# Performance work log

Measured on AMD Instinct MI355X. Metric: run time of the kernel, lower is better.

The kernel has to match this reference:

```python
import jax, jax.numpy as jnp
import numpy as np

LEAKY_SLOPE = 0.01  # torch nn.LeakyReLU default

def leaky_relu(x):
    return jnp.where(x >= 0, x, LEAKY_SLOPE * x)

def setup_inputs() -> dict:
    key = jax.random.key(0)
    ks = jax.random.split(key, 11)
    B, F, C_IN, H, K, D = 2048, 512, 3, 64, 8, 128  # batch, features, expand, layer_conf[0], bucket_num, bucket_dim
    ASR, MM, OUT = 128, 768, 256
    proj_in = ASR + MM + F * D
    inp = {
        "stat_features": jax.random.uniform(ks[0], (B, F), dtype=jnp.float32),
        "asr_embeddings": jax.random.normal(ks[1], (B, ASR), dtype=jnp.float32),
        "mm_embeddings": jax.random.normal(ks[2], (B, MM), dtype=jnp.float32),
        "linear1_w": jax.random.normal(ks[3], (F, C_IN, H), dtype=jnp.float32) * (1.0 / np.sqrt(C_IN)),
        "linear1_b": jax.random.normal(ks[4], (F, 1, H), dtype=jnp.float32),
        "linear2_w": jax.random.normal(ks[5], (F, H, K), dtype=jnp.float32) * (1.0 / np.sqrt(H)),
        "linear2_b": jax.random.normal(ks[6], (F, 1, K), dtype=jnp.float32),
        "tau": jnp.ones((F, 1, K), dtype=jnp.float32),
        "emb": jax.random.normal(ks[7], (F, K, D), dtype=jnp.float32),
        "proj_w": jax.random.normal(ks[8], (OUT, proj_in), dtype=jnp.float32) * (1.0 / np.sqrt(proj_in)),
        "proj_b": jax.random.normal(ks[9], (OUT,), dtype=jnp.float32) * 0.01,
    }
    return inp

def reference(stat_features, asr_embeddings, mm_embeddings,
              linear1_w, linear1_b, linear2_w, linear2_b, tau, emb,
              proj_w, proj_b):
    # sanitize: NaN -> 0, negatives -> 0
    x = stat_features
    x = jnp.where(jnp.isnan(x) | (x < 0.0), 0.0, x)  # [B, F]

    # auto_dis: per-feature tiny MLP. x is expanded to 3 identical copies -> [B,F,1,3]
    # matmul with [F,3,H] == einsum over the 3 copies.
    B, F = x.shape
    x3 = jnp.broadcast_to(x[:, :, None], (B, F, 3))           # [B,F,3]
    h = jnp.einsum('bfc,fch->bfh', x3, linear1_w) + linear1_b[:, 0, :]  # [B,F,H]
    h = jnp.where(h >= 0, h, LEAKY_SLOPE * h)
    s = jnp.einsum('bfh,fhk->bfk', h, linear2_w) + linear2_b[:, 0, :]   # [B,F,K]
    s = jnp.where(s >= 0, s, LEAKY_SLOPE * s)
    s = s * tau[:, 0, :]
    p = jax.nn.softmax(s, axis=-1)                            # [B,F,K]
    y = jnp.einsum('bfk,fkd->bfd', p, emb)                    # [B,F,D]
    y = y.reshape(B, -1)                                      # [B, F*D] (fc = Identity)

    z = jnp.concatenate([asr_embeddings, mm_embeddings, y], axis=1)
    out = jax.nn.relu(z @ proj_w.T + proj_b)                  # [B, 256]
    return out
```

## Files before the change

kernel.cpp:

```cpp
#include <hip/hip_runtime.h>
#include <hip/hip_bf16.h>
#include <math.h>

#define LEAKY 0.01f
#define B_    2048
#define F_    512
#define H_    64
#define K_    8
#define D_    128
#define ASR_  128
#define MM_   768
#define OUT_  256
#define PROJ_IN 66432
#define ZK    4992
#define NSPLIT 8


typedef unsigned short u16;
typedef u16   u16x8 __attribute__((ext_vector_type(8)));
typedef short s16x8 __attribute__((ext_vector_type(8)));
typedef float f32x4 __attribute__((ext_vector_type(4)));

__device__ __forceinline__ u16 f2bf(float x) {
  unsigned int u = __float_as_uint(x);
  u += 0x7fffu + ((u >> 16) & 1u);
  return (u16)(u >> 16);
}

#define PRODUCER_BLOCKS (512 + 1024 + 896 + 224)
#define PWS 132

__global__ __launch_bounds__(256) void producer_kernel(
    const float* __restrict__ stat, const float* __restrict__ w1,
    const float* __restrict__ b1v, const float* __restrict__ w2,
    const float* __restrict__ b2v, const float* __restrict__ tauv,
    const float* __restrict__ pw, const float* __restrict__ emb,
    const float* __restrict__ asr, const float* __restrict__ mm,
    u16* __restrict__ A0, u16* __restrict__ Pf, u16* __restrict__ Wn) {
  __shared__ __align__(16) char smem[15616];
  const int bid = blockIdx.x;
  const int t = threadIdx.x;

  if (bid < 512) {
    const int f0 = (bid >> 3) * 8;
    const int o0 = (bid & 7) * 32;
    float* s_pw = (float*)smem;
    const int fl = t >> 5, k = (t >> 2) & 7, dq = t & 3;
    float4 e[8];
    {
      const float* ep = emb + ((size_t)(f0 + fl) * 8 + k) * 128 + dq * 32;
      #pragma unroll
      for (int j = 0; j < 8; ++j) e[j] = *(const float4*)(ep + j * 4);
    }
    const int cf = t >> 5, cd = (t & 31) * 4;
    const float* pwbase = pw + 896 + (size_t)f0 * 128 + (size_t)(o0)*PROJ_IN + t * 4;
    float4 nxt = *(const float4*)(pwbase);
    for (int r = 0; r < 32; ++r) {
      float* buf = s_pw + (r & 1) * (8 * PWS);
      *(float4*)(buf + cf * PWS + cd) = nxt;
      __syncthreads();
      if (r + 1 < 32) nxt = *(const float4*)(pwbase + (size_t)(r + 1) * PROJ_IN);
      const float* pp = buf + fl * PWS + dq * 32;
      float g = 0.f;
      #pragma unroll
      for (int j = 0; j < 8; ++j) {
        float4 p4 = *(const float4*)(pp + j * 4);
        g = fmaf(e[j].x, p4.x, g);
        g = fmaf(e[j].y, p4.y, g);
        g = fmaf(e[j].z, p4.z, g);
        g = fmaf(e[j].w, p4.w, g);
      }
      g += __shfl_xor(g, 1);
      g += __shfl_xor(g, 2);
      if (dq == 0)
        Wn[(size_t)(o0 + r) * ZK + 896 + (f0 + fl) * 8 + k] = f2bf(g);
    }
  } else if (bid < 1536) {
    const int pb = bid - 512;
    const int f0 = (pb & 127) * 4;
    const int b0 = (pb >> 7) * 256;
    float* s_w1s = (float*)(smem);
    float* s_b1  = (float*)(smem + 1024);
    float* s_w2  = (float*)(smem + 2048);
    float* s_b2  = (float*)(smem + 10240);
    float* s_tau = (float*)(smem + 10368);
    float* s_x   = (float*)(smem + 10496);
    {
      int fl = t >> 6, h = t & 63;
      const float* wf = w1 + (size_t)(f0 + fl) * 192;
      s_w1s[fl * 64 + h] = wf[h] + wf[64 + h] + wf[128 + h];
      s_b1[fl * 64 + h] = b1v[(size_t)(f0 + fl) * 64 + h];
    }
    for (int i = t; i < 4 * 512; i += 256) {
      int fl = i >> 9, idx = i & 511;
      s_w2[fl * 512 + idx] = w2[(size_t)(f0 + fl) * 512 + idx];
    }
    if (t < 32) {
      s_b2[t]  = b2v[f0 * 8 + t];
      s_tau[t] = tauv[f0 * 8 + t];
    }
    for (int p = 0; p < 4; ++p) {
      int i = p * 256 + t;
      int r = i >> 2, fl = i & 3;
      float v = stat[(size_t)(b0 + r) * F_ + f0 + fl];
      s_x[r * 5 + fl] = (v >= 0.f) ? v : 0.f;
    }
    __syncthreads();

    const int w = t >> 6;
    const int lane = t & 63;
    const float* w1p = s_w1s + w * 64;
    const float* b1p = s_b1 + w * 64;
    const float* w2p = s_w2 + w * 512;
    float x[4];
    #pragma unroll
    for (int p = 0; p < 4; ++p) x[p] = s_x[(lane + 64 * p) * 5 + w];
    float acc[4][8] = {{0.f}};
    #pragma unroll 4
    for (int i = 0; i < 64; ++i) {
      float wv = w1p[i], bv = b1p[i];
      float4 wa = *(const float4*)(w2p + i * 8);
      float4 wb = *(const float4*)(w2p + i * 8 + 4);
      #pragma unroll
      for (int p = 0; p < 4; ++p) {
        float h0 = fmaf(x[p], wv, bv);
        float h = fmaf(LEAKY, fminf(h0, 0.f), fmaxf(h0, 0.f));
        acc[p][0] = fmaf(h, wa.x, acc[p][0]);
        acc[p][1] = fmaf(h, wa.y, acc[p][1]);
        acc[p][2] = fmaf(h, wa.z, acc[p][2]);
        acc[p][3] = fmaf(h, wa.w, acc[p][3]);
        acc[p][4] = fmaf(h, wb.x, acc[p][4]);
        acc[p][5] = fmaf(h, wb.y, acc[p][5]);
        acc[p][6] = fmaf(h, wb.z, acc[p][6]);
        acc[p][7] = fmaf(h, wb.w, acc[p][7]);
      }
    }
    #pragma unroll
    for (int p = 0; p < 4; ++p) {
      float s[K_];
      float m = -1e30f;
      #pragma unroll
      for (int kk = 0; kk < K_; ++kk) {
        float v = acc[p][kk] + s_b2[w * 8 + kk];
        v = (v >= 0.f) ? v : LEAKY * v;
        v *= s_tau[w * 8 + kk];
        s[kk] = v;
        m = fmaxf(m, v);
      }
      float sum = 0.f;
      #pragma unroll
      for (int kk = 0; kk < K_; ++kk) { s[kk] = __expf(s[kk] - m); sum += s[kk]; }
      float inv = 1.f / sum;
      u16x8 hv;
      #pragma unroll
      for (int kk = 0; kk < K_; ++kk) hv[kk] = f2bf(s[kk] * inv);
      *(u16x8*)(Pf + ((size_t)(f0 + w) * B_ + b0 + lane + 64 * p) * 8) = hv;
    }
  } else if (bid < 2432) {
    const int item = bid - 1536;
    const int cidx = item * 256 + t;
    const int r = cidx / 112, c = cidx % 112;
    float4 v0, v1;
    if (c < 16) {
      const float* s = asr + (size_t)r * ASR_ + c * 8;
      v0 = *(const float4*)(s); v1 = *(const float4*)(s + 4);
    } else {
      const float* s = mm + (size_t)r * MM_ + (c - 16) * 8;
      v0 = *(const float4*)(s); v1 = *(const float4*)(s + 4);
    }
    u16x8 hv = {f2bf(v0.x), f2bf(v0.y), f2bf(v0.z), f2bf(v0.w),
                f2bf(v1.x), f2bf(v1.y), f2bf(v1.z), f2bf(v1.w)};
    *(u16x8*)(A0 + (size_t)r * 896 + c * 8) = hv;
  } else {
    const int item = bid - 2432;
    #pragma unroll
    for (int rr = 0; rr < 4; ++rr) {
      int idx = item * 1024 + rr * 256 + t;
      int o = idx / 896, j = idx % 896;
      Wn[(size_t)o * ZK + j] = f2bf(pw[(size_t)o * PROJ_IN + j]);
    }
  }
}

#define SAS 72
__global__ __launch_bounds__(256) void gemm_kernel(
    const u16* __restrict__ A0, const u16* __restrict__ Pf,
    const u16* __restrict__ Wn, float* __restrict__ part) {
  const int bm0 = blockIdx.x * 64;
  const int bn0 = blockIdx.y * 64;
  const int kz  = blockIdx.z;
  const int it0 = kz * 10;
  const int itn = (kz == 7) ? 8 : 10;
  __shared__ u16 sA[64 * SAS];
  __shared__ u16 sB[64 * SAS];
  const int t = threadIdx.x;
  const int w = t >> 6, L = t & 63;
  const int l16 = L & 15, q8 = (L >> 4) * 8;
  const int wm = (w >> 1) * 32, wn = (w & 1) * 32;
  const int row = t >> 2, lk = t & 3;
  const int pp = t >> 5, pg = t & 31;
  f32x4 acc[2][2] = {{{0.f,0.f,0.f,0.f},{0.f,0.f,0.f,0.f}},
                     {{0.f,0.f,0.f,0.f},{0.f,0.f,0.f,0.f}}};
  u16x8 ra[2], rb[2];

#define LOAD_TILES(IT)                                                        \
  {                                                                           \
    const int k0_ = (IT) * 64;                                                \
    if (k0_ < 896) {                                                          \
      const u16* s_ = A0 + (size_t)(bm0 + row) * 896 + k0_ + lk * 8;          \
      ra[0] = *(const u16x8*)(s_);                                            \
      ra[1] = *(const u16x8*)(s_ + 32);                                       \
    } else {                                                                  \
      const int fb_ = (k0_ - 896) >> 3;                                       \
      const u16* s_ = Pf + ((size_t)(fb_ + pp) * B_ + bm0 + pg) * 8;          \
      ra[0] = *(const u16x8*)(s_);                                            \
      ra[1] = *(const u16x8*)(s_ + 256);                        \
    }                                                                         \
    const u16* sb_ = Wn + (size_t)(bn0 + row) * ZK + k0_ + lk * 8;            \
    rb[0] = *(const u16x8*)(sb_);                                             \
    rb[1] = *(const u16x8*)(sb_ + 32);                                        \
  }

#define STORE_TILES(IT)                                                       \
  {                                                                           \
    if ((IT) * 64 < 896) {                                                    \
      *(u16x8*)&sA[row * SAS + lk * 8]      = ra[0];                          \
      *(u16x8*)&sA[row * SAS + lk * 8 + 32] = ra[1];                          \
    } else {                                                                  \
      *(u16x8*)&sA[pg * SAS + pp * 8]        = ra[0];                         \
      *(u16x8*)&sA[(pg + 32) * SAS + pp * 8] = ra[1];                         \
    }                                                                         \
    *(u16x8*)&sB[row * SAS + lk * 8]      = rb[0];                            \
    *(u16x8*)&sB[row * SAS + lk * 8 + 32] = rb[1];                            \
  }

  LOAD_TILES(it0);
  for (int it = it0; it < it0 + itn; ++it) {
    __syncthreads();
    STORE_TILES(it);
    __syncthreads();
    if (it + 1 < it0 + itn) LOAD_TILES(it + 1);
    #pragma unroll
    for (int ks = 0; ks < 2; ++ks) {
      s16x8 a0 = *(const s16x8*)&sA[(wm + l16) * SAS + ks * 32 + q8];
      s16x8 a1 = *(const s16x8*)&sA[(wm + 16 + l16) * SAS + ks * 32 + q8];
      s16x8 b0 = *(const s16x8*)&sB[(wn + l16) * SAS + ks * 32 + q8];
      s16x8 b1 = *(const s16x8*)&sB[(wn + 16 + l16) * SAS + ks * 32 + q8];
      acc[0][0] = __builtin_amdgcn_mfma_f32_16x16x32_bf16(a0, b0, acc[0][0], 0, 0, 0);
      acc[0][1] = __builtin_amdgcn_mfma_f32_16x16x32_bf16(a0, b1, acc[0][1], 0, 0, 0);
      acc[1][0] = __builtin_amdgcn_mfma_f32_16x16x32_bf16(a1, b0, acc[1][0], 0, 0, 0);
      acc[1][1] = __builtin_amdgcn_mfma_f32_16x16x32_bf16(a1, b1, acc[1][1], 0, 0, 0);
    }
  }
#undef LOAD_TILES
#undef STORE_TILES

  float* dst = part + (size_t)kz * B_ * OUT_;
  #pragma unroll
  for (int mf = 0; mf < 2; ++mf) {
    const int r0 = bm0 + wm + mf * 16 + (L >> 4) * 4;
    #pragma unroll
    for (int nf = 0; nf < 2; ++nf) {
      const int col = bn0 + wn + nf * 16 + l16;
      #pragma unroll
      for (int i = 0; i < 4; ++i)
        dst[(size_t)(r0 + i) * OUT_ + col] = acc[mf][nf][i];
    }
  }
}

__global__ __launch_bounds__(256) void combine_kernel(
    const float* __restrict__ part, const float* __restrict__ pb,
    float* __restrict__ out) {
  const int idx4 = (blockIdx.x * 256 + threadIdx.x) * 4;
  const int o = idx4 & (OUT_ - 1);
  float4 bv = *(const float4*)(pb + o);
  float4 r = bv;
  #pragma unroll
  for (int kz = 0; kz < NSPLIT; ++kz) {
    float4 a = *(const float4*)(part + (size_t)kz * B_ * OUT_ + idx4);
    r.x += a.x; r.y += a.y; r.z += a.z; r.w += a.w;
  }
  r.x = r.x > 0.f ? r.x : 0.f;
  r.y = r.y > 0.f ? r.y : 0.f;
  r.z = r.z > 0.f ? r.z : 0.f;
  r.w = r.w > 0.f ? r.w : 0.f;
  *(float4*)(out + idx4) = r;
}

extern "C" void kernel_launch(void* const* d_in, const int* in_sizes, int n_in,
                              void* d_out, int out_size, void* d_ws, size_t ws_size,
                              hipStream_t stream) {
  (void)in_sizes; (void)n_in; (void)out_size; (void)ws_size;
  const float* stat = (const float*)d_in[0];
  const float* asr  = (const float*)d_in[1];
  const float* mm   = (const float*)d_in[2];
  const float* w1   = (const float*)d_in[3];
  const float* b1   = (const float*)d_in[4];
  const float* w2   = (const float*)d_in[5];
  const float* b2   = (const float*)d_in[6];
  const float* tau  = (const float*)d_in[7];
  const float* emb  = (const float*)d_in[8];
  const float* pw   = (const float*)d_in[9];
  const float* pb   = (const float*)d_in[10];
  float* out = (float*)d_out;
  char* ws = (char*)d_ws;
  u16*   A0   = (u16*)(ws);
  u16*   Pf   = (u16*)(ws + 3670016);
  u16*   Wn   = (u16*)(ws + 20447232);
  float* part = (float*)(ws + 23003136);

  producer_kernel<<<PRODUCER_BLOCKS, 256, 0, stream>>>(
      stat, w1, b1, w2, b2, tau, pw, emb, asr, mm, A0, Pf, Wn);
  gemm_kernel<<<dim3(B_ / 64, OUT_ / 64, NSPLIT), 256, 0, stream>>>(
      A0, Pf, Wn, part);
  combine_kernel<<<B_ * OUT_ / 1024, 256, 0, stream>>>(part, pb, out);
}
```

Before: 161.6 us.

## Load projection weights directly to registers and read w2 via scalar loads

The emb-times-proj-weight folding branch no longer stages proj_w rows through double-buffered shared memory with a barrier per row. Each thread now loads its own 32-float slice straight from global memory into two register buffers, alternating between them, and reduces across the quad with DPP instead of shuffles. The auto_dis branch reads w2, b2 and tau through wave-uniform pointers (readfirstlane) so they can become scalar loads rather than shared-memory copies, and loads stat as one float4 per thread. This removes barriers and LDS traffic, at the cost of higher register pressure and less coalesced global reads in the first branch.

```diff
diff --git a/kernel.cpp b/kernel.cpp
--- a/kernel.cpp
+++ b/kernel.cpp
@@ -27,8 +27,31 @@
   return (u16)(u >> 16);
 }
 
+__device__ __forceinline__ float quad_sum(float g) {
+  int a = __builtin_amdgcn_update_dpp(0, __float_as_int(g), 0xB1, 0xF, 0xF, true);
+  g += __int_as_float(a);
+  int b = __builtin_amdgcn_update_dpp(0, __float_as_int(g), 0x4E, 0xF, 0xF, true);
+  return g + __int_as_float(b);
+}
+
+__device__ __forceinline__ void ldrow(float4 (&b)[8], const float* p) {
+  #pragma unroll
+  for (int j = 0; j < 8; ++j) b[j] = *(const float4*)(p + j * 4);
+}
+
+__device__ __forceinline__ float dot32(const float4 (&b)[8], const float4 (&e)[8]) {
+  float gp0 = 0.f, gp1 = 0.f;
+  #pragma unroll
+  for (int j = 0; j < 8; ++j) {
+    gp0 = fmaf(e[j].x, b[j].x, gp0);
+    gp1 = fmaf(e[j].y, b[j].y, gp1);
+    gp0 = fmaf(e[j].z, b[j].z, gp0);
+    gp1 = fmaf(e[j].w, b[j].w, gp1);
+  }
+  return gp0 + gp1;
+}
+
 #define PRODUCER_BLOCKS (512 + 1024 + 896 + 224)
-#define PWS 132
 
 __global__ __launch_bounds__(256) void producer_kernel(
     const float* __restrict__ stat, const float* __restrict__ w1,
@@ -44,7 +67,6 @@
   if (bid < 512) {
     const int f0 = (bid >> 3) * 8;
     const int o0 = (bid & 7) * 32;
-    float* s_pw = (float*)smem;
     const int fl = t >> 5, k = (t >> 2) & 7, dq = t & 3;
     float4 e[8];
     {
@@ -52,28 +74,25 @@
       #pragma unroll
       for (int j = 0; j < 8; ++j) e[j] = *(const float4*)(ep + j * 4);
     }
-    const int cf = t >> 5, cd = (t & 31) * 4;
-    const float* pwbase = pw + 896 + (size_t)f0 * 128 + (size_t)(o0)*PROJ_IN + t * 4;
-    float4 nxt = *(const float4*)(pwbase);
-    for (int r = 0; r < 32; ++r) {
-      float* buf = s_pw + (r & 1) * (8 * PWS);
-      *(float4*)(buf + cf * PWS + cd) = nxt;
-      __syncthreads();
-      if (r + 1 < 32) nxt = *(const float4*)(pwbase + (size_t)(r + 1) * PROJ_IN);
-      const float* pp = buf + fl * PWS + dq * 32;
-      float g = 0.f;
-      #pragma unroll
-      for (int j = 0; j < 8; ++j) {
-        float4 p4 = *(const float4*)(pp + j * 4);
-        g = fmaf(e[j].x, p4.x, g);
-        g = fmaf(e[j].y, p4.y, g);
-        g = fmaf(e[j].z, p4.z, g);
-        g = fmaf(e[j].w, p4.w, g);
+    const float* gsrc = pw + 896 + (size_t)(f0 + fl) * 128 + dq * 32
+                        + (size_t)o0 * PROJ_IN;
+    u16* wdst = Wn + 896 + (size_t)(f0 + fl) * 8 + k;
+    float4 bufA[8], bufB[8];
+    ldrow(bufA, gsrc);
+    #pragma unroll
+    for (int rr2 = 0; rr2 < 16; ++rr2) {
+      const int r0 = 2 * rr2;
+      ldrow(bufB, gsrc + (size_t)(r0 + 1) * PROJ_IN);
+      {
+        float g = quad_sum(dot32(bufA, e));
+        if (dq == 0) wdst[(size_t)(o0 + r0) * ZK] = f2bf(g);
       }
-      g += __shfl_xor(g, 1);
-      g += __shfl_xor(g, 2);
-      if (dq == 0)
-        Wn[(size_t)(o0 + r) * ZK + 896 + (f0 + fl) * 8 + k] = f2bf(g);
+      if (r0 + 2 < 32)
+        ldrow(bufA, gsrc + (size_t)(r0 + 2) * PROJ_IN);
+      {
+        float g = quad_sum(dot32(bufB, e));
+        if (dq == 0) wdst[(size_t)(o0 + r0 + 1) * ZK] = f2bf(g);
+      }
     }
   } else if (bid < 1536) {
     const int pb = bid - 512;
@@ -81,37 +100,31 @@
     const int b0 = (pb >> 7) * 256;
     float* s_w1s = (float*)(smem);
     float* s_b1  = (float*)(smem + 1024);
-    float* s_w2  = (float*)(smem + 2048);
-    float* s_b2  = (float*)(smem + 10240);
-    float* s_tau = (float*)(smem + 10368);
-    float* s_x   = (float*)(smem + 10496);
+    float* s_x   = (float*)(smem + 2048);
     {
       int fl = t >> 6, h = t & 63;
       const float* wf = w1 + (size_t)(f0 + fl) * 192;
       s_w1s[fl * 64 + h] = wf[h] + wf[64 + h] + wf[128 + h];
       s_b1[fl * 64 + h] = b1v[(size_t)(f0 + fl) * 64 + h];
     }
-    for (int i = t; i < 4 * 512; i += 256) {
-      int fl = i >> 9, idx = i & 511;
-      s_w2[fl * 512 + idx] = w2[(size_t)(f0 + fl) * 512 + idx];
-    }
-    if (t < 32) {
-      s_b2[t]  = b2v[f0 * 8 + t];
-      s_tau[t] = tauv[f0 * 8 + t];
-    }
-    for (int p = 0; p < 4; ++p) {
-      int i = p * 256 + t;
-      int r = i >> 2, fl = i & 3;
-      float v = stat[(size_t)(b0 + r) * F_ + f0 + fl];
-      s_x[r * 5 + fl] = (v >= 0.f) ? v : 0.f;
+    {
+      float4 sv = *(const float4*)(stat + (size_t)(b0 + t) * F_ + f0);
+      float* xr_ = s_x + t * 5;
+      xr_[0] = (sv.x >= 0.f) ? sv.x : 0.f;
+      xr_[1] = (sv.y >= 0.f) ? sv.y : 0.f;
+      xr_[2] = (sv.z >= 0.f) ? sv.z : 0.f;
+      xr_[3] = (sv.w >= 0.f) ? sv.w : 0.f;
     }
     __syncthreads();
 
     const int w = t >> 6;
+    const int wu = __builtin_amdgcn_readfirstlane(w);
     const int lane = t & 63;
     const float* w1p = s_w1s + w * 64;
     const float* b1p = s_b1 + w * 64;
-    const float* w2p = s_w2 + w * 512;
+    const float* w2u  = w2   + (size_t)(f0 + wu) * 512;
+    const float* b2u  = b2v  + (size_t)(f0 + wu) * 8;
+    const float* tauu = tauv + (size_t)(f0 + wu) * 8;
     float x[4];
     #pragma unroll
     for (int p = 0; p < 4; ++p) x[p] = s_x[(lane + 64 * p) * 5 + w];
@@ -119,8 +132,8 @@
     #pragma unroll 4
     for (int i = 0; i < 64; ++i) {
       float wv = w1p[i], bv = b1p[i];
-      float4 wa = *(const float4*)(w2p + i * 8);
-      float4 wb = *(const float4*)(w2p + i * 8 + 4);
+      float4 wa = *(const float4*)(w2u + i * 8);
+      float4 wb = *(const float4*)(w2u + i * 8 + 4);
       #pragma unroll
       for (int p = 0; p < 4; ++p) {
         float h0 = fmaf(x[p], wv, bv);
@@ -141,9 +154,9 @@
       float m = -1e30f;
       #pragma unroll
       for (int kk = 0; kk < K_; ++kk) {
-        float v = acc[p][kk] + s_b2[w * 8 + kk];
+        float v = acc[p][kk] + b2u[kk];
         v = (v >= 0.f) ? v : LEAKY * v;
-        v *= s_tau[w * 8 + kk];
+        v *= tauu[kk];
         s[kk] = v;
         m = fmaxf(m, v);
       }
```

Result: slower. 188.2 us (+16.4%).
